# Optimization experiments

Hardware: AMD Instinct MI355X
Metric: run time of the kernel (lower is better)

## Reference

```python
import jax, jax.numpy as jnp
import numpy as np

B, C, H, W = 4, 256, 64, 64
CI = 3
TEMPERATURE = 0.0001 * 5
EPS = 2.220446049250313e-16  # sys.float_info.epsilon


def _nearest_up4(x):
    # nn.Upsample(scale_factor=4, mode='nearest'): [B,C,H,W] -> [B,C,4H,4W]
    return jnp.repeat(jnp.repeat(x, 4, axis=2), 4, axis=3)


def _avg_pool2(x):
    # AvgPool2d(kernel=2, stride=2, pad=0)
    b, c, h, w = x.shape
    return x.reshape(b, c, h // 2, 2, w // 2, 2).mean(axis=(3, 5))


def _center_norm(feats):
    # subtract per-channel spatial mean, then L2-normalize over channels per position
    b, c, h, w = feats.shape
    t = feats.reshape(b, c, h * w)
    t = t - t.mean(axis=-1, keepdims=True)
    n = jnp.linalg.norm(t, axis=1, keepdims=True) + EPS
    return t / n  # [B,C,HW]


def setup_inputs() -> dict:
    key = jax.random.key(0)
    k1, k2, k3 = jax.random.split(key, 3)
    return {
        "x_feats": jax.random.normal(k1, (B, C, H, W), jnp.float32),
        "y_feats": jax.random.normal(k2, (B, C, H, W), jnp.float32),
        "y_img": jax.random.uniform(k3, (B, CI, 4 * H, 4 * W), jnp.float32),
    }


def reference(x_feats, y_feats, y_img):
    b, c, h, w = x_feats.shape
    hw = h * w
    theta = _center_norm(x_feats)  # [B,C,HW]
    phi = _center_norm(y_feats)    # [B,C,HW]
    f = jnp.einsum('bcm,bcn->bmn', theta, phi)  # dense correlation [B,HW,HW]
    loss_feat_pair = jnp.mean(jnp.abs(theta - phi))  # F.l1_loss(theta, phi)
    # WTA_scale_weight == 1 -> WTA branch bypassed, just temperature scaling
    f_wta = f / TEMPERATURE
    f_div_c = jax.nn.softmax(f_wta, axis=-1)  # [B,HW,HW]
    # warped features: f_div_C @ y_feats^T
    b_lab = y_feats.reshape(b, c, hw)
    y = jnp.einsum('bmn,bcn->bcm', f_div_c, b_lab).reshape(b, c, h, w)
    # soft-argmax coordinates
    xc = (jnp.arange(hw) % w).astype(x_feats.dtype)   # [HW]
    yc = (jnp.arange(hw) // w).astype(x_feats.dtype)  # [HW]
    coords_x = f_div_c @ xc  # [B,HW]
    coords_y = f_div_c @ yc  # [B,HW]
    coords1 = jnp.stack([coords_x, coords_y], axis=1).reshape(b, 2, h, w)
    coords0 = jnp.stack([xc, yc], axis=0).reshape(1, 2, h, w)
    flow = _nearest_up4(coords1 - coords0)  # [B,2,4H,4W]
    # image warping branch (y_img is not None)
    yi = _avg_pool2(_avg_pool2(y_img))  # [B,CI,H,W]
    ci = yi.shape[1]
    yi_flat = yi.reshape(b, ci, hw)
    y_img_attn = jnp.einsum('bmn,bcn->bmc', f_div_c, yi_flat)  # [B,HW,CI]
    f_div_c_v = jax.nn.softmax(jnp.swapaxes(f_wta, 1, 2), axis=-1)
    y_img_cyc = jnp.einsum('bmn,bnc->bcm', f_div_c_v, y_img_attn).reshape(b, ci, h, w)
    y_img_out = jnp.swapaxes(y_img_attn, 1, 2).reshape(b, ci, h, w)
    return (y, flow, _nearest_up4(y_img_out), _nearest_up4(y_img_cyc), loss_feat_pair)
```

## Files before the change

kernel.cpp:

```cpp
#include <hip/hip_runtime.h>
#include <math.h>

#define HW   4096
#define NCH  256
#define NB   4

constexpr float TEMP  = (float)(0.0001 * 5.0);
constexpr float INV_T = 1.0f / TEMP;
constexpr float EPSN  = 2.220446049250313e-16f;

typedef __attribute__((ext_vector_type(8))) _Float16 f16x8;
typedef __attribute__((ext_vector_type(4))) _Float16 f16x4;
typedef __attribute__((ext_vector_type(4))) float    f32x4;

constexpr size_t OFF_YT    = 0;
constexpr size_t OFF_YI    = OFF_YT    + (size_t)NB*HW*NCH;
constexpr size_t OFF_MEAN  = OFF_YI    + (size_t)NB*3*HW;
constexpr size_t OFF_RNORM = OFF_MEAN  + (size_t)2*NB*NCH;
constexpr size_t OFF_NSQP  = OFF_RNORM + (size_t)2*NB*HW;
constexpr size_t OFF_F     = OFF_NSQP  + (size_t)2*NB*8*HW;
constexpr size_t OFF_YP    = OFF_F     + (size_t)HW*HW;
constexpr size_t OFF_ROWP  = OFF_YP;
constexpr size_t OFF_COLP  = OFF_YP + (size_t)32*7*HW;
constexpr size_t OFF_RMAX  = OFF_YP    + (size_t)8*NCH*HW;
constexpr size_t OFF_RSUM  = OFF_RMAX  + HW;
constexpr size_t OFF_CMAX  = OFF_RSUM  + HW;
constexpr size_t OFF_CSUM  = OFF_CMAX  + HW;
constexpr size_t OFF_COORD = OFF_CSUM  + HW;
constexpr size_t OFF_ATTN  = OFF_COORD + (size_t)NB*2*HW;
constexpr size_t OFF_CYC   = OFF_ATTN  + (size_t)NB*HW*3;
constexpr size_t OFF_CYCP  = OFF_CYC   + (size_t)NB*3*HW;
constexpr size_t OFF_LOSSP = OFF_CYCP  + (size_t)32*3*HW;
constexpr size_t OFF_F16   = OFF_LOSSP + 1024;

constexpr size_t OUT_Y    = 0;
constexpr size_t OUT_FLOW = (size_t)NB*NCH*HW;
constexpr size_t OUT_IMG  = OUT_FLOW + (size_t)NB*2*256*256;
constexpr size_t OUT_CYCO = OUT_IMG  + (size_t)NB*3*256*256;
constexpr size_t OUT_LOSS = OUT_CYCO + (size_t)NB*3*256*256;

__device__ __forceinline__ void gload16(const void* g, void* l) {
    __builtin_amdgcn_global_load_lds(
        (const __attribute__((address_space(1))) unsigned int*)g,
        (__attribute__((address_space(3))) unsigned int*)l, 16, 0, 0);
}

__global__ void mean_kernel(const float* __restrict__ xf, const float* __restrict__ yf,
                            float* __restrict__ means) {
    const float* src = (blockIdx.y == 0 ? xf : yf) + (size_t)blockIdx.x * HW;
    float s = 0.f;
    for (int i = threadIdx.x; i < HW; i += 256) s += src[i];
    __shared__ float red[256];
    red[threadIdx.x] = s; __syncthreads();
    for (int st = 128; st > 0; st >>= 1) {
        if (threadIdx.x < st) red[threadIdx.x] += red[threadIdx.x + st];
        __syncthreads();
    }
    if (threadIdx.x == 0) means[blockIdx.y * (NB*NCH) + blockIdx.x] = red[0] * (1.0f / HW);
}

__global__ void nsq_combine_kernel(const float* __restrict__ part, float* __restrict__ rnorms,
                                   int b) {
    int t = blockIdx.y;
    int m = blockIdx.x * 256 + threadIdx.x;
    const float* p = part + ((size_t)t*NB + b) * 8 * HW + m;
    float s = 0.f;
    for (int k = 0; k < 8; ++k) s += p[(size_t)k * HW];
    rnorms[((size_t)t*NB + b) * HW + m] = 1.0f / (sqrtf(s) + EPSN);
}

__global__ void ycast_kernel(const float* __restrict__ yf, _Float16* __restrict__ yf16) {
    size_t i = ((size_t)blockIdx.x * 256 + threadIdx.x) * 8;
    const float4* s = (const float4*)(yf + i);
    float4 v0 = s[0], v1 = s[1];
    f16x8 o;
    o[0]=(_Float16)v0.x; o[1]=(_Float16)v0.y; o[2]=(_Float16)v0.z; o[3]=(_Float16)v0.w;
    o[4]=(_Float16)v1.x; o[5]=(_Float16)v1.y; o[6]=(_Float16)v1.z; o[7]=(_Float16)v1.w;
    *(f16x8*)(yf16 + i) = o;
}

__global__ void prep_kernel(const float* __restrict__ xf, const float* __restrict__ yf,
                            const float* __restrict__ means,
                            _Float16* __restrict__ th, _Float16* __restrict__ tl,
                            _Float16* __restrict__ ph, _Float16* __restrict__ pl,
                            float* __restrict__ nsqp, int b) {
    __shared__ float tile[32][33];
    __shared__ float sqr[8][33];
    int t = blockIdx.z;
    int c0 = blockIdx.x * 32, m0 = blockIdx.y * 32;
    const float* src = (t == 0 ? xf : yf) + (size_t)b * NCH * HW;
    const float* mn  = means + t * (NB*NCH) + b * NCH;
    int tx = threadIdx.x & 31, ty = threadIdx.x >> 5;
    float sq = 0.f;
    for (int i = ty; i < 32; i += 8) {
        float v = src[(size_t)(c0 + i) * HW + m0 + tx] - mn[c0 + i];
        tile[i][tx] = v;
        sq += v * v;
    }
    sqr[ty][tx] = sq;
    __syncthreads();
    _Float16* H = (t == 0 ? th : ph);
    _Float16* L = (t == 0 ? tl : pl);
    for (int i = ty; i < 32; i += 8) {
        float v = tile[tx][i];
        _Float16 h = (_Float16)v;
        _Float16 l = (_Float16)(v - (float)h);
        H[(size_t)(m0 + i)*NCH + c0 + tx] = h;
        L[(size_t)(m0 + i)*NCH + c0 + tx] = l;
    }
    if (ty == 0) {
        float s = 0.f;
        #pragma unroll
        for (int k = 0; k < 8; ++k) s += sqr[k][tx];
        nsqp[(((size_t)t*NB + b) * 8 + blockIdx.x) * HW + m0 + tx] = s;
    }
}

__global__ void avgpool_kernel(const float* __restrict__ yimg, float* __restrict__ yi) {
    size_t idx = (size_t)blockIdx.x * 256 + threadIdx.x;
    int m  = (int)(idx & (HW - 1));
    int bc = (int)(idx >> 12);
    int h = m >> 6, w = m & 63;
    const float* p = yimg + (size_t)bc * 65536 + (size_t)(h*4) * 256 + w*4;
    float s = 0.f;
    #pragma unroll
    for (int dy = 0; dy < 4; ++dy) {
        #pragma unroll
        for (int dx = 0; dx < 4; ++dx) s += p[dy*256 + dx];
    }
    yi[idx] = s * (1.0f/16.0f);
}

__global__ __launch_bounds__(256) void gemm_f_kernel(
        const _Float16* __restrict__ th, const _Float16* __restrict__ tl,
        const _Float16* __restrict__ ph, const _Float16* __restrict__ pl,
        const float* __restrict__ rnorms, const float* __restrict__ yi,
        float* __restrict__ f, float* __restrict__ rowp, float* __restrict__ colp,
        int b) {
    __shared__ char lds[2][4][8192];
    int tid  = threadIdx.x;
    int lane = tid & 63;
    int w = tid >> 6, wm = w >> 1, wn = w & 1;
    int m0 = blockIdx.y * 128, n0 = blockIdx.x * 128;

    int o0 = tid * 16, o1 = o0 + 4096;
    int r0 = o0 >> 6, s0 = (o0 >> 4) & 3, g0 = s0 ^ ((r0 >> 1) & 3);
    int r1 = o1 >> 6, s1 = (o1 >> 4) & 3, g1 = s1 ^ ((r1 >> 1) & 3);
    size_t ga0 = (size_t)(n0 + r0)*NCH + g0*8;
    size_t ga1 = (size_t)(n0 + r1)*NCH + g1*8;
    size_t gb0 = (size_t)(m0 + r0)*NCH + g0*8;
    size_t gb1 = (size_t)(m0 + r1)*NCH + g1*8;

    int fra = wm*64 + (lane & 15);
    int frb = wn*64 + (lane & 15);
    int ks  = lane >> 4;

    auto STAGE = [&](int buf, int k0) {
        gload16(ph + ga0 + k0, &lds[buf][0][o0]);
        gload16(ph + ga1 + k0, &lds[buf][0][o1]);
        gload16(pl + ga0 + k0, &lds[buf][1][o0]);
        gload16(pl + ga1 + k0, &lds[buf][1][o1]);
        gload16(th + gb0 + k0, &lds[buf][2][o0]);
        gload16(th + gb1 + k0, &lds[buf][2][o1]);
        gload16(tl + gb0 + k0, &lds[buf][3][o0]);
        gload16(tl + gb1 + k0, &lds[buf][3][o1]);
    };

    f32x4 acc[4][4];
    #pragma unroll
    for (int i = 0; i < 4; ++i)
        #pragma unroll
        for (int j = 0; j < 4; ++j) acc[i][j] = (f32x4){0.f, 0.f, 0.f, 0.f};

    STAGE(0, 0);
    __syncthreads();
    int cur = 0;
    for (int kt = 0; kt < 8; ++kt) {
        if (kt < 7) STAGE(cur ^ 1, (kt + 1) * 32);

        f16x8 ah[4], al[4], bh[4], bl[4];
        #pragma unroll
        for (int i = 0; i < 4; ++i) {
            int rowa = fra + i*16;
            int offa = rowa*64 + ((ks ^ ((rowa >> 1) & 3)) << 4);
            ah[i] = *(const f16x8*)&lds[cur][0][offa];
            al[i] = *(const f16x8*)&lds[cur][1][offa];
            int rowb = frb + i*16;
            int offb = rowb*64 + ((ks ^ ((rowb >> 1) & 3)) << 4);
            bh[i] = *(const f16x8*)&lds[cur][2][offb];
            bl[i] = *(const f16x8*)&lds[cur][3][offb];
        }
        #pragma unroll
        for (int i = 0; i < 4; ++i)
            #pragma unroll
            for (int j = 0; j < 4; ++j) {
                acc[i][j] = __builtin_amdgcn_mfma_f32_16x16x32_f16(ah[i], bh[j], acc[i][j], 0, 0, 0);
                acc[i][j] = __builtin_amdgcn_mfma_f32_16x16x32_f16(ah[i], bl[j], acc[i][j], 0, 0, 0);
                acc[i][j] = __builtin_amdgcn_mfma_f32_16x16x32_f16(al[i], bh[j], acc[i][j], 0, 0, 0);
            }
        __syncthreads();
        cur ^= 1;
    }

    const float* rnx = rnorms + (size_t)b * HW;
    const float* rny = rnorms + (size_t)(NB + b) * HW;
    int mg[4];  float rxv[4];
    #pragma unroll
    for (int j = 0; j < 4; ++j) {
        mg[j] = m0 + wn*64 + j*16 + (lane & 15);
        rxv[j] = rnx[mg[j]];
    }
    int nl0 = wm*64 + (lane >> 4)*4;
    #pragma unroll
    for (int i = 0; i < 4; ++i)
        #pragma unroll
        for (int r = 0; r < 4; ++r) {
            float ry = rny[n0 + nl0 + i*16 + r];
            #pragma unroll
            for (int j = 0; j < 4; ++j) acc[i][j][r] *= rxv[j] * ry;
        }

    #pragma unroll
    for (int j = 0; j < 4; ++j)
        #pragma unroll
        for (int i = 0; i < 4; ++i)
            *(f32x4*)&f[(size_t)mg[j]*HW + n0 + nl0 + i*16] = acc[i][j];

    float* S     = (float*)&lds[0][0][0];
    float* rowm  = S;
    float* sums6 = S + 256;
    float* colm  = S + 1792;
    float* colsm = S + 2048;

    #pragma unroll
    for (int j = 0; j < 4; ++j) {
        float v = acc[0][j][0];
        #pragma unroll
        for (int i = 0; i < 4; ++i)
            #pragma unroll
            for (int r = 0; r < 4; ++r) v = fmaxf(v, acc[i][j][r]);
        v = fmaxf(v, __shfl_xor(v, 16));
        v = fmaxf(v, __shfl_xor(v, 32));
        if ((lane >> 4) == 0) rowm[wm*128 + wn*64 + j*16 + lane] = v;
    }
    #pragma unroll
    for (int i = 0; i < 4; ++i)
        #pragma unroll
        for (int r = 0; r < 4; ++r) {
            float v = fmaxf(fmaxf(acc[i][0][r], acc[i][1][r]),
                            fmaxf(acc[i][2][r], acc[i][3][r]));
            #pragma unroll
            for (int d = 1; d < 16; d <<= 1) v = fmaxf(v, __shfl_xor(v, d));
            if ((lane & 15) == 0) colm[wn*128 + wm*64 + i*16 + (lane >> 4)*4 + r] = v;
        }
    __syncthreads();

    float bm[4];
    #pragma unroll
    for (int j = 0; j < 4; ++j) {
        int ml = wn*64 + j*16 + (lane & 15);
        bm[j] = fmaxf(rowm[ml], rowm[128 + ml]);
    }
    float a6[4][6];
    #pragma unroll
    for (int j = 0; j < 4; ++j)
        #pragma unroll
        for (int q = 0; q < 6; ++q) a6[j][q] = 0.f;
    const float* yib = yi + (size_t)b * 3 * HW;
    #pragma unroll
    for (int i = 0; i < 4; ++i)
        #pragma unroll
        for (int r = 0; r < 4; ++r) {
            int ng = n0 + nl0 + i*16 + r;
            float xc = (float)(ng & 63), yc = (float)(ng >> 6);
            float y0 = yib[ng], y1 = yib[HW + ng], y2 = yib[2*HW + ng];
            #pragma unroll
            for (int j = 0; j < 4; ++j) {
                float e = __expf((acc[i][j][r] - bm[j]) * INV_T);
                a6[j][0] += e;      a6[j][1] += e*xc; a6[j][2] += e*yc;
                a6[j][3] += e*y0;   a6[j][4] += e*y1; a6[j][5] += e*y2;
            }
        }
    #pragma unroll
    for (int j = 0; j < 4; ++j)
        #pragma unroll
        for (int q = 0; q < 6; ++q) {
            float v = a6[j][q];
            v += __shfl_xor(v, 16);
            v += __shfl_xor(v, 32);
            if ((lane >> 4) == 0) sums6[(wm*128 + wn*64 + j*16 + lane)*6 + q] = v;
        }
    #pragma unroll
    for (int i = 0; i < 4; ++i)
        #pragma unroll
        for (int r = 0; r < 4; ++r) {
            int nl = wm*64 + i*16 + (lane >> 4)*4 + r;
            float cm = fmaxf(colm[nl], colm[128 + nl]);
            float cs = 0.f;
            #pragma unroll
            for (int j = 0; j < 4; ++j) cs += __expf((acc[i][j][r] - cm) * INV_T);
            #pragma unroll
            for (int d = 1; d < 16; d <<= 1) cs += __shfl_xor(cs, d);
            if ((lane & 15) == 0) colsm[wn*128 + nl] = cs;
        }
    __syncthreads();

    if (tid < 128) {
        int ml = tid;
        float m2 = fmaxf(rowm[ml], rowm[128 + ml]);
        rowp[((size_t)blockIdx.x*7 + 0)*HW + m0 + ml] = m2;
        #pragma unroll
        for (int q = 0; q < 6; ++q)
            rowp[((size_t)blockIdx.x*7 + 1 + q)*HW + m0 + ml] =
                sums6[ml*6 + q] + sums6[(128 + ml)*6 + q];
    } else {
        int nl = tid - 128;
        float c2 = fmaxf(colm[nl], colm[128 + nl]);
        colp[((size_t)blockIdx.y*2 + 0)*HW + n0 + nl] = c2;
        colp[((size_t)blockIdx.y*2 + 1)*HW + n0 + nl] = colsm[nl] + colsm[128 + nl];
    }
}

__global__ void rowcol_combine_kernel(const float* __restrict__ rowp,
        const float* __restrict__ colp,
        float* __restrict__ rmax, float* __restrict__ rsuminv,
        float* __restrict__ coords, float* __restrict__ attn,
        float* __restrict__ cmax, float* __restrict__ csuminv, int b) {
    int idx = blockIdx.x * 256 + threadIdx.x;
    if (blockIdx.y == 0) {
        int m = idx;
        float gm = -3.0e38f;
        for (int t = 0; t < 32; ++t) gm = fmaxf(gm, rowp[((size_t)t*7)*HW + m]);
        float S=0, CX=0, CY=0, A0=0, A1=0, A2=0;
        for (int t = 0; t < 32; ++t) {
            const float* p = rowp + (size_t)t*7*HW + m;
            float wgt = __expf((p[0] - gm) * INV_T);
            S  += p[1*HW] * wgt; CX += p[2*HW] * wgt; CY += p[3*HW] * wgt;
            A0 += p[4*HW] * wgt; A1 += p[5*HW] * wgt; A2 += p[6*HW] * wgt;
        }
        float inv = 1.0f / S;
        rmax[m] = gm; rsuminv[m] = inv;
        coords[((size_t)b*2 + 0)*HW + m] = CX * inv;
        coords[((size_t)b*2 + 1)*HW + m] = CY * inv;
        attn[((size_t)b*HW + m)*3 + 0] = A0 * inv;
        attn[((size_t)b*HW + m)*3 + 1] = A1 * inv;
        attn[((size_t)b*HW + m)*3 + 2] = A2 * inv;
    } else {
        int n = idx;
        float gm = -3.0e38f;
        for (int t = 0; t < 32; ++t) gm = fmaxf(gm, colp[((size_t)t*2)*HW + n]);
        float S = 0.f;
        for (int t = 0; t < 32; ++t) {
            const float* p = colp + (size_t)t*2*HW + n;
            S += p[1*HW] * __expf((p[0] - gm) * INV_T);
        }
        cmax[n] = gm;
        csuminv[n] = 1.0f / S;
    }
}

__global__ __launch_bounds__(512) void gemm_y_kernel(const float* __restrict__ f,
        const float* __restrict__ rmax, const _Float16* __restrict__ yf16,
        _Float16* __restrict__ yph, int b) {
    __shared__ __align__(16) char ldsA[4096];
    __shared__ __align__(16) char ldsB[16384];
    int tid  = threadIdx.x;
    int lane = tid & 63;
    int w = tid >> 6, wm = w >> 2, wn = w & 3;
    int m0 = blockIdx.x * 64;
    int ks = blockIdx.y;
    const _Float16* Yb = yf16 + (size_t)b * NCH * HW;

    int ar = (tid & 255) >> 2, akc = tid & 3;
    int aoff = ar*64 + ((akc ^ ((ar >> 1) & 3)) << 4);
    float arm = rmax[m0 + ar];
    const float* frow = f + (size_t)(m0 + ar)*HW + akc*8;

    int o0 = tid*16, o1 = o0 + 8192;
    int br0 = o0 >> 6, bs0 = (o0 >> 4) & 3, bg0 = bs0 ^ ((br0 >> 1) & 3);
    int br1 = o1 >> 6, bs1 = (o1 >> 4) & 3, bg1 = bs1 ^ ((br1 >> 1) & 3);
    size_t gb0 = (size_t)br0*HW + bg0*8;
    size_t gb1 = (size_t)br1*HW + bg1*8;

    int fra = wm*32 + (lane & 15);
    int frb = wn*64 + (lane & 15);
    int kslot = lane >> 4;

    f32x4 acc[2][4];
    #pragma unroll
    for (int i = 0; i < 2; ++i)
        #pragma unroll
        for (int j = 0; j < 4; ++j) acc[i][j] = (f32x4){0.f, 0.f, 0.f, 0.f};

    for (int k0 = ks*1024; k0 < ks*1024 + 1024; k0 += 32) {
        gload16(Yb + gb0 + k0, &ldsB[o0]);
        gload16(Yb + gb1 + k0, &ldsB[o1]);
        if (tid < 256) {
            const float4* fp = (const float4*)(frow + k0);
            float4 v0 = fp[0], v1 = fp[1];
            f16x8 pk;
            pk[0] = (_Float16)__expf((v0.x - arm) * INV_T);
            pk[1] = (_Float16)__expf((v0.y - arm) * INV_T);
            pk[2] = (_Float16)__expf((v0.z - arm) * INV_T);
            pk[3] = (_Float16)__expf((v0.w - arm) * INV_T);
            pk[4] = (_Float16)__expf((v1.x - arm) * INV_T);
            pk[5] = (_Float16)__expf((v1.y - arm) * INV_T);
            pk[6] = (_Float16)__expf((v1.z - arm) * INV_T);
            pk[7] = (_Float16)__expf((v1.w - arm) * INV_T);
            *(f16x8*)&ldsA[aoff] = pk;
        }
        __syncthreads();

        f16x8 af[2], bf[4];
        #pragma unroll
        for (int i = 0; i < 2; ++i) {
            int rowa = fra + i*16;
            af[i] = *(const f16x8*)&ldsA[rowa*64 + ((kslot ^ ((rowa >> 1) & 3)) << 4)];
        }
        #pragma unroll
        for (int j = 0; j < 4; ++j) {
            int rowb = frb + j*16;
            bf[j] = *(const f16x8*)&ldsB[rowb*64 + ((kslot ^ ((rowb >> 1) & 3)) << 4)];
        }
        #pragma unroll
        for (int i = 0; i < 2; ++i)
            #pragma unroll
            for (int j = 0; j < 4; ++j)
                acc[i][j] = __builtin_amdgcn_mfma_f32_16x16x32_f16(af[i], bf[j], acc[i][j], 0, 0, 0);
        __syncthreads();
    }

    #pragma unroll
    for (int i = 0; i < 2; ++i) {
        int m = m0 + wm*32 + i*16 + (lane >> 4) * 4;
        #pragma unroll
        for (int j = 0; j < 4; ++j) {
            int c = wn*64 + j*16 + (lane & 15);
            f16x4 v;
            #pragma unroll
            for (int r = 0; r < 4; ++r) v[r] = (_Float16)acc[i][j][r];
            *(f16x4*)(yph + ((size_t)ks*NCH + c)*HW + m) = v;
        }
    }
}

__global__ void ycombine_kernel(const _Float16* __restrict__ yph, const float* __restrict__ rsuminv,
                                float* __restrict__ out, int b) {
    size_t idx = (size_t)blockIdx.x * 256 + threadIdx.x;
    int m = (int)(idx & (HW - 1));
    float s = 0.f;
    #pragma unroll
    for (int k = 0; k < 4; ++k) s += (float)yph[(size_t)k*NCH*HW + idx];
    out[OUT_Y + (size_t)b*NCH*HW + idx] = s * rsuminv[m];
}

__global__ __launch_bounds__(256) void cyc_partial_kernel(const float* __restrict__ f,
        const float* __restrict__ cmax, const float* __restrict__ attn,
        float* __restrict__ part, int b) {
    __shared__ float at[128*3];
    int i  = blockIdx.x * 256 + threadIdx.x;
    int j0 = blockIdx.y * 128;
    for (int k = threadIdx.x; k < 384; k += 256)
        at[k] = attn[((size_t)b*HW + j0)*3 + k];
    __syncthreads();
    float cm = cmax[i];
    float a0=0, a1=0, a2=0;
    for (int jj = 0; jj < 128; ++jj) {
        float e = __expf((f[(size_t)(j0+jj)*HW + i] - cm) * INV_T);
        a0 = fmaf(e, at[jj*3+0], a0);
        a1 = fmaf(e, at[jj*3+1], a1);
        a2 = fmaf(e, at[jj*3+2], a2);
    }
    part[((size_t)blockIdx.y*3 + 0)*HW + i] = a0;
    part[((size_t)blockIdx.y*3 + 1)*HW + i] = a1;
    part[((size_t)blockIdx.y*3 + 2)*HW + i] = a2;
}

__global__ void cyc_combine_kernel(const float* __restrict__ part, const float* __restrict__ csuminv,
                                   float* __restrict__ cyc, int b) {
    int i = blockIdx.x * 256 + threadIdx.x;
    int c = blockIdx.y;
    float s = 0.f;
    for (int k = 0; k < 32; ++k) s += part[((size_t)k*3 + c)*HW + i];
    cyc[((size_t)b*3 + c)*HW + i] = s * csuminv[i];
}

__global__ void flow_kernel(const float* __restrict__ coords, float* __restrict__ out) {
    size_t idx = (size_t)blockIdx.x * 256 + threadIdx.x;
    int x4 = (int)(idx & 255);
    int y4 = (int)((idx >> 8) & 255);
    int ch = (int)((idx >> 16) & 1);
    int b  = (int)(idx >> 17);
    int w = x4 >> 2, h = y4 >> 2;
    int m = h*64 + w;
    float c1 = coords[((size_t)b*2 + ch)*HW + m];
    float c0 = (ch == 0) ? (float)w : (float)h;
    out[OUT_FLOW + idx] = c1 - c0;
}

__global__ void imgout_kernel(const float* __restrict__ attn, const float* __restrict__ cyc,
                              float* __restrict__ out) {
    size_t idx = (size_t)blockIdx.x * 256 + threadIdx.x;
    int x4 = (int)(idx & 255);
    int y4 = (int)((idx >> 8) & 255);
    int rest = (int)(idx >> 16);
    int ch = rest % 3, b = rest / 3;
    int m = (y4 >> 2)*64 + (x4 >> 2);
    out[OUT_IMG  + idx] = attn[((size_t)b*HW + m)*3 + ch];
    out[OUT_CYCO + idx] = cyc[((size_t)b*3 + ch)*HW + m];
}

__global__ void loss_partial_kernel(const float* __restrict__ xf, const float* __restrict__ yf,
                                    const float* __restrict__ means, const float* __restrict__ rnorms,
                                    float* __restrict__ part) {
    __shared__ float red[256];
    size_t base = (size_t)blockIdx.x * 4096;
    float s = 0.f;
    for (int k = 0; k < 16; ++k) {
        size_t id = base + (size_t)k*256 + threadIdx.x;
        int m  = (int)(id & (HW - 1));
        int bc = (int)(id >> 12);
        int b  = bc >> 8;
        float th = (xf[id] - means[bc])          * rnorms[(size_t)b*HW + m];
        float ph = (yf[id] - means[NB*NCH + bc]) * rnorms[(size_t)(NB + b)*HW + m];
        s += fabsf(th - ph);
    }
    red[threadIdx.x] = s; __syncthreads();
    for (int st = 128; st > 0; st >>= 1) {
        if (threadIdx.x < st) red[threadIdx.x] += red[threadIdx.x + st];
        __syncthreads();
    }
    if (threadIdx.x == 0) part[blockIdx.x] = red[0];
}

__global__ void loss_final_kernel(const float* __restrict__ part, float* __restrict__ out) {
    __shared__ float red[256];
    float s = 0.f;
    for (int k = threadIdx.x; k < 1024; k += 256) s += part[k];
    red[threadIdx.x] = s; __syncthreads();
    for (int st = 128; st > 0; st >>= 1) {
        if (threadIdx.x < st) red[threadIdx.x] += red[threadIdx.x + st];
        __syncthreads();
    }
    if (threadIdx.x == 0) out[OUT_LOSS] = red[0] * (1.0f / 4194304.0f);
}

extern "C" void kernel_launch(void* const* d_in, const int* in_sizes, int n_in,
                              void* d_out, int out_size, void* d_ws, size_t ws_size,
                              hipStream_t stream) {
    (void)in_sizes; (void)n_in; (void)out_size; (void)ws_size;
    const float* xf   = (const float*)d_in[0];
    const float* yf   = (const float*)d_in[1];
    const float* yimg = (const float*)d_in[2];
    float* out = (float*)d_out;
    float* ws  = (float*)d_ws;

    _Float16* yf16 = (_Float16*)(ws + OFF_YT);
    float* yi      = ws + OFF_YI;
    float* means   = ws + OFF_MEAN;
    float* rnorms  = ws + OFF_RNORM;
    float* nsqp    = ws + OFF_NSQP;
    float* fbuf    = ws + OFF_F;
    _Float16* yph  = (_Float16*)(ws + OFF_YP);
    float* rowp    = ws + OFF_ROWP;
    float* colp    = ws + OFF_COLP;
    float* rmax    = ws + OFF_RMAX;
    float* rsuminv = ws + OFF_RSUM;
    float* cmax    = ws + OFF_CMAX;
    float* csuminv = ws + OFF_CSUM;
    float* coords  = ws + OFF_COORD;
    float* attn    = ws + OFF_ATTN;
    float* cyc     = ws + OFF_CYC;
    float* cycp    = ws + OFF_CYCP;
    float* lossp   = ws + OFF_LOSSP;
    _Float16* th = (_Float16*)(ws + OFF_F16);
    _Float16* tl = th + (size_t)HW*NCH;
    _Float16* ph = tl + (size_t)HW*NCH;
    _Float16* pl = ph + (size_t)HW*NCH;

    mean_kernel        <<<dim3(NB*NCH, 2),   256, 0, stream>>>(xf, yf, means);
    ycast_kernel       <<<2048,              256, 0, stream>>>(yf, yf16);
    avgpool_kernel     <<<NB*3*HW/256,       256, 0, stream>>>(yimg, yi);

    for (int b = 0; b < NB; ++b) {
        prep_kernel          <<<dim3(8, 128, 2), 256, 0, stream>>>(xf, yf, means, th, tl, ph, pl,
                                                                   nsqp, b);
        nsq_combine_kernel   <<<dim3(16, 2),     256, 0, stream>>>(nsqp, rnorms, b);
        gemm_f_kernel        <<<dim3(32, 32),    256, 0, stream>>>(th, tl, ph, pl, rnorms, yi,
                                                                   fbuf, rowp, colp, b);
        rowcol_combine_kernel<<<dim3(16, 2),     256, 0, stream>>>(rowp, colp, rmax, rsuminv,
                                                                   coords, attn, cmax, csuminv, b);
        gemm_y_kernel        <<<dim3(64, 4),     512, 0, stream>>>(fbuf, rmax, yf16, yph, b);
        ycombine_kernel      <<<NCH*HW/256,      256, 0, stream>>>(yph, rsuminv, out, b);
        cyc_partial_kernel   <<<dim3(16, 32),    256, 0, stream>>>(fbuf, cmax, attn, cycp, b);
        cyc_combine_kernel   <<<dim3(16, 3),     256, 0, stream>>>(cycp, csuminv, cyc, b);
    }

    flow_kernel        <<<NB*2*65536/256, 256, 0, stream>>>(coords, out);
    imgout_kernel      <<<NB*3*65536/256, 256, 0, stream>>>(attn, cyc, out);
    loss_partial_kernel<<<1024,           256, 0, stream>>>(xf, yf, means, rnorms, lossp);
    loss_final_kernel  <<<1,              256, 0, stream>>>(lossp, out);
}
```

Baseline: 527.9 us.

## Move column-softmax denominator into cyc pass, spread exp work, add MFMA priority

The column-sum exp reduction is removed from the F GEMM epilogue and its combine kernel. The cyc partial pass now accumulates the denominator alongside the weighted sums, reusing the exps it already computes. The Y GEMM's A-tile exp conversion is spread across all 512 threads (4 elements each) instead of 256 threads doing 8. s_setprio is raised around the MFMA loops in both GEMMs. The result is fewer exp evaluations and less epilogue work in the F GEMM, at the cost of one extra partial buffer to write and read.

```diff
diff --git a/kernel.cpp b/kernel.cpp
--- a/kernel.cpp
+++ b/kernel.cpp
@@ -25,12 +25,11 @@
 constexpr size_t OFF_RMAX  = OFF_YP    + (size_t)8*NCH*HW;
 constexpr size_t OFF_RSUM  = OFF_RMAX  + HW;
 constexpr size_t OFF_CMAX  = OFF_RSUM  + HW;
-constexpr size_t OFF_CSUM  = OFF_CMAX  + HW;
-constexpr size_t OFF_COORD = OFF_CSUM  + HW;
+constexpr size_t OFF_COORD = OFF_CMAX  + HW;
 constexpr size_t OFF_ATTN  = OFF_COORD + (size_t)NB*2*HW;
 constexpr size_t OFF_CYC   = OFF_ATTN  + (size_t)NB*HW*3;
 constexpr size_t OFF_CYCP  = OFF_CYC   + (size_t)NB*3*HW;
-constexpr size_t OFF_LOSSP = OFF_CYCP  + (size_t)32*3*HW;
+constexpr size_t OFF_LOSSP = OFF_CYCP  + (size_t)32*4*HW;
 constexpr size_t OFF_F16   = OFF_LOSSP + 1024;
 
 constexpr size_t OUT_Y    = 0;
@@ -190,6 +189,7 @@
             bh[i] = *(const f16x8*)&lds[cur][2][offb];
             bl[i] = *(const f16x8*)&lds[cur][3][offb];
         }
+        __builtin_amdgcn_s_setprio(1);
         #pragma unroll
         for (int i = 0; i < 4; ++i)
             #pragma unroll
@@ -198,6 +198,7 @@
                 acc[i][j] = __builtin_amdgcn_mfma_f32_16x16x32_f16(ah[i], bl[j], acc[i][j], 0, 0, 0);
                 acc[i][j] = __builtin_amdgcn_mfma_f32_16x16x32_f16(al[i], bh[j], acc[i][j], 0, 0, 0);
             }
+        __builtin_amdgcn_s_setprio(0);
         __syncthreads();
         cur ^= 1;
     }
@@ -230,7 +231,6 @@
     float* rowm  = S;
     float* sums6 = S + 256;
     float* colm  = S + 1792;
-    float* colsm = S + 2048;
 
     #pragma unroll
     for (int j = 0; j < 4; ++j) {
@@ -290,19 +290,6 @@
             v += __shfl_xor(v, 32);
             if ((lane >> 4) == 0) sums6[(wm*128 + wn*64 + j*16 + lane)*6 + q] = v;
         }
-    #pragma unroll
-    for (int i = 0; i < 4; ++i)
-        #pragma unroll
-        for (int r = 0; r < 4; ++r) {
-            int nl = wm*64 + i*16 + (lane >> 4)*4 + r;
-            float cm = fmaxf(colm[nl], colm[128 + nl]);
-            float cs = 0.f;
-            #pragma unroll
-            for (int j = 0; j < 4; ++j) cs += __expf((acc[i][j][r] - cm) * INV_T);
-            #pragma unroll
-            for (int d = 1; d < 16; d <<= 1) cs += __shfl_xor(cs, d);
-            if ((lane & 15) == 0) colsm[wn*128 + nl] = cs;
-        }
     __syncthreads();
 
     if (tid < 128) {
@@ -315,9 +302,7 @@
                 sums6[ml*6 + q] + sums6[(128 + ml)*6 + q];
     } else {
         int nl = tid - 128;
-        float c2 = fmaxf(colm[nl], colm[128 + nl]);
-        colp[((size_t)blockIdx.y*2 + 0)*HW + n0 + nl] = c2;
-        colp[((size_t)blockIdx.y*2 + 1)*HW + n0 + nl] = colsm[nl] + colsm[128 + nl];
+        colp[(size_t)blockIdx.y*HW + n0 + nl] = fmaxf(colm[nl], colm[128 + nl]);
     }
 }
 
@@ -325,7 +310,7 @@
         const float* __restrict__ colp,
         float* __restrict__ rmax, float* __restrict__ rsuminv,
         float* __restrict__ coords, float* __restrict__ attn,
-        float* __restrict__ cmax, float* __restrict__ csuminv, int b) {
+        float* __restrict__ cmax, int b) {
     int idx = blockIdx.x * 256 + threadIdx.x;
     if (blockIdx.y == 0) {
         int m = idx;
@@ -348,14 +333,8 @@
     } else {
         int n = idx;
         float gm = -3.0e38f;
-        for (int t = 0; t < 32; ++t) gm = fmaxf(gm, colp[((size_t)t*2)*HW + n]);
-        float S = 0.f;
-        for (int t = 0; t < 32; ++t) {
-            const float* p = colp + (size_t)t*2*HW + n;
-            S += p[1*HW] * __expf((p[0] - gm) * INV_T);
-        }
+        for (int t = 0; t < 32; ++t) gm = fmaxf(gm, colp[(size_t)t*HW + n]);
         cmax[n] = gm;
-        csuminv[n] = 1.0f / S;
     }
 }
 
@@ -371,10 +350,11 @@
     int ks = blockIdx.y;
     const _Float16* Yb = yf16 + (size_t)b * NCH * HW;
 
-    int ar = (tid & 255) >> 2, akc = tid & 3;
-    int aoff = ar*64 + ((akc ^ ((ar >> 1) & 3)) << 4);
+    int ar = tid >> 3, kc = tid & 7;
+    int aslot = kc >> 1, ahalf = kc & 1;
+    int aoff = ar*64 + ((aslot ^ ((ar >> 1) & 3)) << 4) + ahalf*8;
     float arm = rmax[m0 + ar];
-    const float* frow = f + (size_t)(m0 + ar)*HW + akc*8;
+    const float* frow = f + (size_t)(m0 + ar)*HW + kc*4;
 
     int o0 = tid*16, o1 = o0 + 8192;
     int br0 = o0 >> 6, bs0 = (o0 >> 4) & 3, bg0 = bs0 ^ ((br0 >> 1) & 3);
@@ -395,19 +375,14 @@
     for (int k0 = ks*1024; k0 < ks*1024 + 1024; k0 += 32) {
         gload16(Yb + gb0 + k0, &ldsB[o0]);
         gload16(Yb + gb1 + k0, &ldsB[o1]);
-        if (tid < 256) {
-            const float4* fp = (const float4*)(frow + k0);
-            float4 v0 = fp[0], v1 = fp[1];
-            f16x8 pk;
-            pk[0] = (_Float16)__expf((v0.x - arm) * INV_T);
-            pk[1] = (_Float16)__expf((v0.y - arm) * INV_T);
-            pk[2] = (_Float16)__expf((v0.z - arm) * INV_T);
-            pk[3] = (_Float16)__expf((v0.w - arm) * INV_T);
-            pk[4] = (_Float16)__expf((v1.x - arm) * INV_T);
-            pk[5] = (_Float16)__expf((v1.y - arm) * INV_T);
-            pk[6] = (_Float16)__expf((v1.z - arm) * INV_T);
-            pk[7] = (_Float16)__expf((v1.w - arm) * INV_T);
-            *(f16x8*)&ldsA[aoff] = pk;
+        {
+            float4 v = *(const float4*)(frow + k0);
+            f16x4 pk;
+            pk[0] = (_Float16)__expf((v.x - arm) * INV_T);
+            pk[1] = (_Float16)__expf((v.y - arm) * INV_T);
+            pk[2] = (_Float16)__expf((v.z - arm) * INV_T);
+            pk[3] = (_Float16)__expf((v.w - arm) * INV_T);
+            *(f16x4*)&ldsA[aoff] = pk;
         }
         __syncthreads();
 
@@ -422,11 +397,13 @@
             int rowb = frb + j*16;
             bf[j] = *(const f16x8*)&ldsB[rowb*64 + ((kslot ^ ((rowb >> 1) & 3)) << 4)];
         }
+        __builtin_amdgcn_s_setprio(1);
         #pragma unroll
         for (int i = 0; i < 2; ++i)
             #pragma unroll
             for (int j = 0; j < 4; ++j)
                 acc[i][j] = __builtin_amdgcn_mfma_f32_16x16x32_f16(af[i], bf[j], acc[i][j], 0, 0, 0);
+        __builtin_amdgcn_s_setprio(0);
         __syncthreads();
     }
 
@@ -464,25 +441,30 @@
         at[k] = attn[((size_t)b*HW + j0)*3 + k];
     __syncthreads();
     float cm = cmax[i];
-    float a0=0, a1=0, a2=0;
+    float a0=0, a1=0, a2=0, a3=0;
     for (int jj = 0; jj < 128; ++jj) {
         float e = __expf((f[(size_t)(j0+jj)*HW + i] - cm) * INV_T);
         a0 = fmaf(e, at[jj*3+0], a0);
         a1 = fmaf(e, at[jj*3+1], a1);
         a2 = fmaf(e, at[jj*3+2], a2);
-    }
-    part[((size_t)blockIdx.y*3 + 0)*HW + i] = a0;
-    part[((size_t)blockIdx.y*3 + 1)*HW + i] = a1;
-    part[((size_t)blockIdx.y*3 + 2)*HW + i] = a2;
-}
-
-__global__ void cyc_combine_kernel(const float* __restrict__ part, const float* __restrict__ csuminv,
+        a3 += e;
+    }
+    part[((size_t)blockIdx.y*4 + 0)*HW + i] = a0;
+    part[((size_t)blockIdx.y*4 + 1)*HW + i] = a1;
+    part[((size_t)blockIdx.y*4 + 2)*HW + i] = a2;
+    part[((size_t)blockIdx.y*4 + 3)*HW + i] = a3;
+}
+
+__global__ void cyc_combine_kernel(const float* __restrict__ part,
                                    float* __restrict__ cyc, int b) {
     int i = blockIdx.x * 256 + threadIdx.x;
     int c = blockIdx.y;
-    float s = 0.f;
-    for (int k = 0; k < 32; ++k) s += part[((size_t)k*3 + c)*HW + i];
-    cyc[((size_t)b*3 + c)*HW + i] = s * csuminv[i];
+    float s = 0.f, den = 0.f;
+    for (int k = 0; k < 32; ++k) {
+        s   += part[((size_t)k*4 + c)*HW + i];
+        den += part[((size_t)k*4 + 3)*HW + i];
+    }
+    cyc[((size_t)b*3 + c)*HW + i] = s / den;
 }
 
 __global__ void flow_kernel(const float* __restrict__ coords, float* __restrict__ out) {
@@ -567,7 +549,6 @@
     float* rmax    = ws + OFF_RMAX;
     float* rsuminv = ws + OFF_RSUM;
     float* cmax    = ws + OFF_CMAX;
-    float* csuminv = ws + OFF_CSUM;
     float* coords  = ws + OFF_COORD;
     float* attn    = ws + OFF_ATTN;
     float* cyc     = ws + OFF_CYC;
@@ -589,11 +570,11 @@
         gemm_f_kernel        <<<dim3(32, 32),    256, 0, stream>>>(th, tl, ph, pl, rnorms, yi,
                                                                    fbuf, rowp, colp, b);
         rowcol_combine_kernel<<<dim3(16, 2),     256, 0, stream>>>(rowp, colp, rmax, rsuminv,
-                                                                   coords, attn, cmax, csuminv, b);
+                                                                   coords, attn, cmax, b);
         gemm_y_kernel        <<<dim3(64, 4),     512, 0, stream>>>(fbuf, rmax, yf16, yph, b);
         ycombine_kernel      <<<NCH*HW/256,      256, 0, stream>>>(yph, rsuminv, out, b);
         cyc_partial_kernel   <<<dim3(16, 32),    256, 0, stream>>>(fbuf, cmax, attn, cycp, b);
-        cyc_combine_kernel   <<<dim3(16, 3),     256, 0, stream>>>(cycp, csuminv, cyc, b);
+        cyc_combine_kernel   <<<dim3(16, 3),     256, 0, stream>>>(cycp, cyc, b);
     }
 
     flow_kernel        <<<NB*2*65536/256, 256, 0, stream>>>(coords, out);
```

Result: no change. 521.4 us (-1.2%).
